# Kernel optimization log

Hardware: AMD Instinct MI355X
Metric: run time of the kernel (lower is better)

The kernel has to match this reference:

```python
import jax, jax.numpy as jnp
import numpy as np

N_NODES = 100000
N_EDGES = 1600000
D = 128


def _gine_layer(x, src, dst, e, W1, b1, W2, b2):
    # message: relu(x_j + e_ji), aggregate: sum at destination
    m = jax.nn.relu(x[src] + e)                       # [E, D]
    agg = jax.ops.segment_sum(m, dst, num_segments=x.shape[0])  # [N, D]
    h = agg + x                                       # (1 + eps) * x_i with eps = 0
    h = jax.nn.relu(jnp.dot(h, W1) + b1)
    return jnp.dot(h, W2) + b2


def setup_inputs() -> dict:
    key = jax.random.key(0)
    ks = jax.random.split(key, 16)
    s = 0.05
    inp = {
        "x": jax.random.normal(ks[0], (N_NODES, D), dtype=jnp.float32),
        "edge_index": jax.random.randint(ks[1], (2, N_EDGES), 0, N_NODES, dtype=jnp.int64) if jax.config.jax_enable_x64 else jax.random.randint(ks[1], (2, N_EDGES), 0, N_NODES, dtype=jnp.int32),
        "edge_attr": jax.random.randint(ks[2], (N_EDGES,), 0, 100, dtype=jnp.int32),
        "edge_emb": jax.random.normal(ks[3], (100, D), dtype=jnp.float32) * s,
        "Win": jax.random.normal(ks[4], (D, D), dtype=jnp.float32) * s,
        "b_in": jnp.zeros((D,), dtype=jnp.float32),
        "W1_0": jax.random.normal(ks[5], (D, D), dtype=jnp.float32) * s,
        "b1_0": jnp.zeros((D,), dtype=jnp.float32),
        "W2_0": jax.random.normal(ks[6], (D, D), dtype=jnp.float32) * s,
        "b2_0": jnp.zeros((D,), dtype=jnp.float32),
        "W1_1": jax.random.normal(ks[7], (D, D), dtype=jnp.float32) * s,
        "b1_1": jnp.zeros((D,), dtype=jnp.float32),
        "W2_1": jax.random.normal(ks[8], (D, D), dtype=jnp.float32) * s,
        "b2_1": jnp.zeros((D,), dtype=jnp.float32),
        "Wout": jax.random.normal(ks[9], (D, 1), dtype=jnp.float32) * s,
        "b_out": jnp.zeros((1,), dtype=jnp.float32),
    }
    return inp


def reference(x, edge_index, edge_attr, edge_emb, Win, b_in,
              W1_0, b1_0, W2_0, b2_0, W1_1, b1_1, W2_1, b2_1,
              Wout, b_out):
    src, dst = edge_index[0], edge_index[1]
    e = edge_emb[edge_attr]                 # [E, D] edge-attribute embedding lookup
    h = jnp.dot(x, Win) + b_in              # input_proj
    # layer 0: GINEConv + residual add + relu (norm=none, dropout off)
    h = jax.nn.relu(_gine_layer(h, src, dst, e, W1_0, b1_0, W2_0, b2_0) + h)
    # layer 1
    h = jax.nn.relu(_gine_layer(h, src, dst, e, W1_1, b1_1, W2_1, b2_1) + h)
    # output_mlp: single Linear(hidden, 1); no final activation, no pooling
    return jnp.dot(h, Wout) + b_out
```

## Files before the change

### kernel.cpp

```cpp
#include <hip/hip_runtime.h>

#define NN 100000
#define D 128
#define CHUNK 4096
#define BCSTRIDE 392

typedef __attribute__((ext_vector_type(8))) short short8;
typedef __attribute__((ext_vector_type(8))) unsigned short ushort8;
typedef __attribute__((ext_vector_type(4))) float f32x4;

__device__ __forceinline__ float4 ld4(const float* p) { return *(const float4*)p; }

__device__ __forceinline__ unsigned short f2bf(float f) {
    unsigned int u = __float_as_uint(f);
    unsigned int r = u + 0x7fffu + ((u >> 16) & 1u);
    return (unsigned short)(r >> 16);
}
__device__ __forceinline__ float bf2f(unsigned short h) {
    return __uint_as_float(((unsigned int)h) << 16);
}
__device__ __forceinline__ float blo(unsigned int u) { return __uint_as_float(u << 16); }
__device__ __forceinline__ float bhi(unsigned int u) { return __uint_as_float(u & 0xffff0000u); }

__device__ __forceinline__ int swz(int r, int c) {
    return r * 128 + ((((c >> 2) ^ (r & 7)) << 2) | (c & 3));
}

__device__ __forceinline__ void coop_gemm8(
    const unsigned int* uT,
    const unsigned short* __restrict__ Whi, const unsigned short* __restrict__ Wlo,
    int wv, int lane, int lr, int q, f32x4 acc[4])
{
    #pragma unroll
    for (int ks = 0; ks < 4; ++ks) {
        short8 ahi[4], alo[4];
        #pragma unroll
        for (int m = 0; m < 4; ++m) {
            const int row = m * 16 + lr;
            const int cb  = ks * 32 + q * 8;
            const uint4 a0 = *(const uint4*)&uT[swz(row, cb)];
            const uint4 a1 = *(const uint4*)&uT[swz(row, cb + 4)];
            const unsigned int w[8] = {a0.x, a0.y, a0.z, a0.w, a1.x, a1.y, a1.z, a1.w};
            #pragma unroll
            for (int j = 0; j < 8; ++j) {
                ahi[m][j] = (short)(w[j] >> 16);
                alo[m][j] = (short)(w[j] & 0xffffu);
            }
        }
        const int base = ((wv * 4 + ks) * 64 + lane) * 8;
        const short8 bhi8 = *(const short8*)&Whi[base];
        const short8 blo8 = *(const short8*)&Wlo[base];
        #pragma unroll
        for (int m = 0; m < 4; ++m) {
            acc[m] = __builtin_amdgcn_mfma_f32_16x16x32_bf16(alo[m], bhi8, acc[m], 0, 0, 0);
            acc[m] = __builtin_amdgcn_mfma_f32_16x16x32_bf16(ahi[m], blo8, acc[m], 0, 0, 0);
            acc[m] = __builtin_amdgcn_mfma_f32_16x16x32_bf16(ahi[m], bhi8, acc[m], 0, 0, 0);
        }
    }
}

__device__ __forceinline__ void gemm_in_body(
    unsigned int* uT, int bid,
    const float* __restrict__ A1,
    const unsigned short* __restrict__ Whi, const unsigned short* __restrict__ Wlo,
    const float* __restrict__ bias,
    unsigned short* __restrict__ out_hi, unsigned short* __restrict__ out_lo, int N)
{
    const int t    = threadIdx.x;
    const int wv   = t >> 6;
    const int lane = t & 63;
    const int lr   = lane & 15;
    const int q    = lane >> 4;
    const int rE   = wv * 8 + (lane >> 3);
    const int cE   = (lane & 7) * 16;
    const int rowE = bid * 64 + rE;

    {
        float v[16];
        if (rowE < N) {
            const int off = rowE * D + cE;
            #pragma unroll
            for (int k = 0; k < 4; ++k) {
                const float4 x = ld4(&A1[off + k * 4]);
                v[k * 4 + 0] = x.x; v[k * 4 + 1] = x.y; v[k * 4 + 2] = x.z; v[k * 4 + 3] = x.w;
            }
        } else {
            #pragma unroll
            for (int j = 0; j < 16; ++j) v[j] = 0.f;
        }
        #pragma unroll
        for (int k = 0; k < 4; ++k) {
            unsigned int pk[4];
            #pragma unroll
            for (int j = 0; j < 4; ++j) {
                const float f = v[k * 4 + j];
                const unsigned int hi = f2bf(f);
                pk[j] = (hi << 16) | f2bf(f - bf2f((unsigned short)hi));
            }
            *(uint4*)&uT[swz(rE, cE + k * 4)] = make_uint4(pk[0], pk[1], pk[2], pk[3]);
        }
    }
    __syncthreads();

    f32x4 acc[4];
    #pragma unroll
    for (int m = 0; m < 4; ++m) acc[m] = (f32x4){0.f, 0.f, 0.f, 0.f};
    coop_gemm8(uT, Whi, Wlo, wv, lane, lr, q, acc);
    __syncthreads();

    {
        const float b = bias[wv * 16 + lr];
        #pragma unroll
        for (int m = 0; m < 4; ++m)
            #pragma unroll
            for (int r = 0; r < 4; ++r)
                uT[swz(m * 16 + q * 4 + r, wv * 16 + lr)] = __float_as_uint(acc[m][r] + b);
    }
    __syncthreads();

    if (rowE < N) {
        const int off = rowE * D + cE;
        unsigned int w[16];
        #pragma unroll
        for (int k = 0; k < 4; ++k) {
            const uint4 a = *(const uint4*)&uT[swz(rE, cE + k * 4)];
            w[k * 4 + 0] = a.x; w[k * 4 + 1] = a.y; w[k * 4 + 2] = a.z; w[k * 4 + 3] = a.w;
        }
        #pragma unroll
        for (int h8 = 0; h8 < 2; ++h8) {
            ushort8 oh, ol;
            #pragma unroll
            for (int j = 0; j < 8; ++j) {
                const float o = __uint_as_float(w[h8 * 8 + j]);
                const unsigned short h = f2bf(o);
                oh[j] = h;
                ol[j] = f2bf(o - bf2f(h));
            }
            *(ushort8*)&out_hi[off + h8 * 8] = oh;
            *(ushort8*)&out_lo[off + h8 * 8] = ol;
        }
    }
}

__global__ __launch_bounds__(256) void setup_all(
    const float* __restrict__ W0, const float* __restrict__ W1,
    const float* __restrict__ W2, const float* __restrict__ W3,
    const float* __restrict__ W4, unsigned short* __restrict__ wp,
    const float* __restrict__ emb, unsigned int* __restrict__ embp,
    int* __restrict__ binTotal)
{
    const int T = blockIdx.x * 256 + threadIdx.x;
    if (T < 5 * D * D) {
        const int w = T / (D * D);
        const int t = T % (D * D);
        const float* W = (w == 0) ? W0 : (w == 1) ? W1 : (w == 2) ? W2 : (w == 3) ? W3 : W4;
        const int j  = t & 7;
        const int L  = (t >> 3) & 63;
        const int ks = (t >> 9) & 3;
        const int nt = t >> 11;
        const float v = W[(ks * 32 + (L >> 4) * 8 + j) * D + nt * 16 + (L & 15)];
        const unsigned short h = f2bf(v);
        unsigned short* hi = wp + (size_t)w * 2 * D * D;
        hi[t] = h;
        hi[D * D + t] = f2bf(v - bf2f(h));
    } else if (T < 5 * D * D + 6400) {
        const int i = T - 5 * D * D;
        embp[i] = (unsigned int)f2bf(emb[i * 2]) | ((unsigned int)f2bf(emb[i * 2 + 1]) << 16);
    } else if (T < 5 * D * D + 6400 + BCSTRIDE) {
        binTotal[T - 5 * D * D - 6400] = 0;
    }
}

__global__ __launch_bounds__(512, 8) void fuse_count_gemm(
    const int* __restrict__ dst, int* __restrict__ blkcnt,
    int* __restrict__ binTotal, int E, int nbins, int csrB,
    const float* __restrict__ A1,
    const unsigned short* __restrict__ Whi, const unsigned short* __restrict__ Wlo,
    const float* __restrict__ bias,
    unsigned short* __restrict__ out_hi, unsigned short* __restrict__ out_lo,
    int N, int gemmBase)
{
    __shared__ __align__(16) unsigned int uT[64 * 128];
    if ((int)blockIdx.x < csrB) {
        int* hist = (int*)uT;
        const int t = threadIdx.x;
        const int i = blockIdx.x;
        for (int k = t; k < nbins; k += 512) hist[k] = 0;
        __syncthreads();
        const int e0 = i * CHUNK;
        const int e1 = min(E, e0 + CHUNK);
        for (int e = e0 + t; e < e1; e += 512) atomicAdd(&hist[dst[e] >> 8], 1);
        __syncthreads();
        for (int k = t; k < nbins; k += 512) {
            const int c = hist[k];
            blkcnt[i * BCSTRIDE + k] = c;
            if (c) atomicAdd(&binTotal[k], c);
        }
    } else {
        gemm_in_body(uT, blockIdx.x - csrB + gemmBase, A1, Whi, Wlo, bias, out_hi, out_lo, N);
    }
}

__global__ __launch_bounds__(512) void bin_scan(
    const int* __restrict__ binTotal, int* __restrict__ binStart,
    int* __restrict__ binCursor, int nbins)
{
    __shared__ int s[512];
    const int t = threadIdx.x;
    const int v = (t < nbins) ? binTotal[t] : 0;
    s[t] = v;
    __syncthreads();
    for (int off = 1; off < 512; off <<= 1) {
        const int x = (t >= off) ? s[t - off] : 0;
        __syncthreads();
        s[t] += x;
        __syncthreads();
    }
    if (t < nbins) { binStart[t] = s[t] - v; binCursor[t] = s[t] - v; }
    if (t == 0)    binStart[nbins] = s[511];
}

__global__ __launch_bounds__(512, 8) void fuse_scatter_gemm(
    const int* __restrict__ src, const int* __restrict__ dst,
    const int* __restrict__ attr, const int* __restrict__ blkcnt,
    int* __restrict__ binCursor, int2* __restrict__ binned, int E, int nbins, int csrB,
    const float* __restrict__ A1,
    const unsigned short* __restrict__ Whi, const unsigned short* __restrict__ Wlo,
    const float* __restrict__ bias,
    unsigned short* __restrict__ out_hi, unsigned short* __restrict__ out_lo,
    int N, int gemmBase)
{
    __shared__ __align__(16) unsigned int uT[64 * 128];
    if ((int)blockIdx.x < csrB) {
        int* cur = (int*)uT;
        const int t = threadIdx.x;
        const int i = blockIdx.x;
        for (int k = t; k < nbins; k += 512) {
            const int c = blkcnt[i * BCSTRIDE + k];
            if (c) cur[k] = atomicAdd(&binCursor[k], c);
        }
        __syncthreads();
        const int e0 = i * CHUNK;
        const int e1 = min(E, e0 + CHUNK);
        for (int e = e0 + t; e < e1; e += 512) {
            const int d = dst[e];
            const int p = atomicAdd(&cur[d >> 8], 1);
            binned[p] = make_int2(src[e] | (attr[e] << 20), d);
        }
    } else {
        gemm_in_body(uT, blockIdx.x - csrB + gemmBase, A1, Whi, Wlo, bias, out_hi, out_lo, N);
    }
}

__global__ __launch_bounds__(512, 8) void fuse_build_gemm(
    const int2* __restrict__ binned, const int* __restrict__ binStart,
    int* __restrict__ rowptr, int* __restrict__ epack, int csrB,
    const float* __restrict__ A1,
    const unsigned short* __restrict__ Whi, const unsigned short* __restrict__ Wlo,
    const float* __restrict__ bias,
    unsigned short* __restrict__ out_hi, unsigned short* __restrict__ out_lo,
    int N, int gemmBase)
{
    __shared__ __align__(16) unsigned int uT[64 * 128];
    if ((int)blockIdx.x < csrB) {
        int* hist = (int*)uT;
        int* scn  = (int*)uT + 256;
        int* curn = (int*)uT + 512;
        const int t = threadIdx.x;
        const int b = blockIdx.x;
        if (t < 256) hist[t] = 0;
        __syncthreads();
        const int ebeg = binStart[b];
        const int eend = binStart[b + 1];
        for (int e = ebeg + t; e < eend; e += 512) atomicAdd(&hist[binned[e].y & 255], 1);
        __syncthreads();
        if (t < 256) scn[t] = hist[t];
        __syncthreads();
        for (int off = 1; off < 256; off <<= 1) {
            int x = 0;
            if (t < 256 && t >= off) x = scn[t - off];
            __syncthreads();
            if (t < 256) scn[t] += x;
            __syncthreads();
        }
        if (t < 256) {
            const int node = b * 256 + t;
            if (node < N) rowptr[node] = ebeg + scn[t];
            curn[t] = ebeg + scn[t] - hist[t];
        }
        __syncthreads();
        for (int e = ebeg + t; e < eend; e += 512) {
            const int2 v = binned[e];
            const int p = atomicAdd(&curn[v.y & 255], 1);
            epack[p] = v.x;
        }
    } else {
        gemm_in_body(uT, blockIdx.x - csrB + gemmBase, A1, Whi, Wlo, bias, out_hi, out_lo, N);
    }
}

template<bool LAST>
__global__ __launch_bounds__(512, 8) void gine_fused(
    const unsigned short* __restrict__ h_hi, const unsigned short* __restrict__ h_lo,
    const int* __restrict__ rowptr, const int* __restrict__ epack,
    const unsigned int* __restrict__ embp,
    const unsigned short* __restrict__ W1hi, const unsigned short* __restrict__ W1lo,
    const float* __restrict__ b1,
    const unsigned short* __restrict__ W2hi, const unsigned short* __restrict__ W2lo,
    const float* __restrict__ b2,
    unsigned short* __restrict__ out_hi, unsigned short* __restrict__ out_lo,
    const float* __restrict__ Wout, const float* __restrict__ bout,
    float* __restrict__ outv, int N)
{
    __shared__ __align__(16) unsigned int uT[64 * 128];
    const int t    = threadIdx.x;
    const int wv   = t >> 6;
    const int lane = t & 63;
    const int lr   = lane & 15;
    const int q    = lane >> 4;
    const int rE   = wv * 8 + (lane >> 3);
    const int cE   = (lane & 7) * 16;
    const int rowE = blockIdx.x * 64 + rE;

    const unsigned int* hu = (const unsigned int*)h_hi;

    for (int i = 0; i < 8; ++i) {
        const int row  = wv * 8 + i;
        const int node = blockIdx.x * 64 + row;
        if (node >= N) break;
        int start = (node == 0) ? 0 : rowptr[node - 1];
        int end   = rowptr[node];
        start = __builtin_amdgcn_readfirstlane(start);
        end   = __builtin_amdgcn_readfirstlane(end);

        float ax = 0.f, ay = 0.f;
        int j = start;

        for (; j < end && (j & 3); ++j) {
            const int p0 = __builtin_amdgcn_readfirstlane(epack[j]);
            const unsigned int u0 = hu[(p0 & 0xFFFFF) * 64 + lane];
            const unsigned int v0 = embp[(p0 >> 20) * 64 + lane];
            ax += fmaxf(blo(u0) + blo(v0), 0.f);
            ay += fmaxf(bhi(u0) + bhi(v0), 0.f);
        }

        for (; j + 7 < end; j += 8) {
            const int4 pk0 = *(const int4*)&epack[j];
            const int4 pk1 = *(const int4*)&epack[j + 4];
            int p[8];
            p[0] = __builtin_amdgcn_readfirstlane(pk0.x);
            p[1] = __builtin_amdgcn_readfirstlane(pk0.y);
            p[2] = __builtin_amdgcn_readfirstlane(pk0.z);
            p[3] = __builtin_amdgcn_readfirstlane(pk0.w);
            p[4] = __builtin_amdgcn_readfirstlane(pk1.x);
            p[5] = __builtin_amdgcn_readfirstlane(pk1.y);
            p[6] = __builtin_amdgcn_readfirstlane(pk1.z);
            p[7] = __builtin_amdgcn_readfirstlane(pk1.w);
            unsigned int u[8], v[8];
            #pragma unroll
            for (int k = 0; k < 8; ++k) u[k] = hu[(p[k] & 0xFFFFF) * 64 + lane];
            #pragma unroll
            for (int k = 0; k < 8; ++k) v[k] = embp[(p[k] >> 20) * 64 + lane];
            #pragma unroll
            for (int k = 0; k < 8; ++k) {
                ax += fmaxf(blo(u[k]) + blo(v[k]), 0.f);
                ay += fmaxf(bhi(u[k]) + bhi(v[k]), 0.f);
            }
        }

        if (j + 3 < end) {
            const int4 pk0 = *(const int4*)&epack[j];
            int p[4];
            p[0] = __builtin_amdgcn_readfirstlane(pk0.x);
            p[1] = __builtin_amdgcn_readfirstlane(pk0.y);
            p[2] = __builtin_amdgcn_readfirstlane(pk0.z);
            p[3] = __builtin_amdgcn_readfirstlane(pk0.w);
            unsigned int u[4], v[4];
            #pragma unroll
            for (int k = 0; k < 4; ++k) u[k] = hu[(p[k] & 0xFFFFF) * 64 + lane];
            #pragma unroll
            for (int k = 0; k < 4; ++k) v[k] = embp[(p[k] >> 20) * 64 + lane];
            #pragma unroll
            for (int k = 0; k < 4; ++k) {
                ax += fmaxf(blo(u[k]) + blo(v[k]), 0.f);
                ay += fmaxf(bhi(u[k]) + bhi(v[k]), 0.f);
            }
            j += 4;
        }

        for (; j < end; ++j) {
            const int p0 = __builtin_amdgcn_readfirstlane(epack[j]);
            const unsigned int u0 = hu[(p0 & 0xFFFFF) * 64 + lane];
            const unsigned int v0 = embp[(p0 >> 20) * 64 + lane];
            ax += fmaxf(blo(u0) + blo(v0), 0.f);
            ay += fmaxf(bhi(u0) + bhi(v0), 0.f);
        }

        *(float2*)&uT[swz(row, 2 * lane)] = make_float2(ax, ay);
    }

    {
        float v[16];
        if (rowE < N) {
            #pragma unroll
            for (int k = 0; k < 4; ++k) {
                const uint4 a = *(const uint4*)&uT[swz(rE, cE + k * 4)];
                v[k * 4 + 0] = __uint_as_float(a.x);
                v[k * 4 + 1] = __uint_as_float(a.y);
                v[k * 4 + 2] = __uint_as_float(a.z);
                v[k * 4 + 3] = __uint_as_float(a.w);
            }
            const int off = rowE * D + cE;
            #pragma unroll
            for (int h8 = 0; h8 < 2; ++h8) {
                const ushort8 hh = *(const ushort8*)&h_hi[off + h8 * 8];
                const ushort8 ll = *(const ushort8*)&h_lo[off + h8 * 8];
                #pragma unroll
                for (int j = 0; j < 8; ++j) v[h8 * 8 + j] += bf2f(hh[j]) + bf2f(ll[j]);
            }
        } else {
            #pragma unroll
            for (int j = 0; j < 16; ++j) v[j] = 0.f;
        }
        #pragma unroll
        for (int k = 0; k < 4; ++k) {
            unsigned int pk[4];
            #pragma unroll
            for (int j = 0; j < 4; ++j) {
                const float f = v[k * 4 + j];
                const unsigned int hi = f2bf(f);
                pk[j] = (hi << 16) | f2bf(f - bf2f((unsigned short)hi));
            }
            *(uint4*)&uT[swz(rE, cE + k * 4)] = make_uint4(pk[0], pk[1], pk[2], pk[3]);
        }
    }
    __syncthreads();

    f32x4 acc[4];
    #pragma unroll
    for (int m = 0; m < 4; ++m) acc[m] = (f32x4){0.f, 0.f, 0.f, 0.f};
    coop_gemm8(uT, W1hi, W1lo, wv, lane, lr, q, acc);
    __syncthreads();

    {
        const float b = b1[wv * 16 + lr];
        #pragma unroll
        for (int m = 0; m < 4; ++m)
            #pragma unroll
            for (int r = 0; r < 4; ++r) {
                const float o = fmaxf(acc[m][r] + b, 0.f);
                const unsigned int hi = f2bf(o);
                const unsigned int lo = f2bf(o - bf2f((unsigned short)hi));
                uT[swz(m * 16 + q * 4 + r, wv * 16 + lr)] = (hi << 16) | lo;
            }
    }
    __syncthreads();

    f32x4 acc2[4];
    #pragma unroll
    for (int m = 0; m < 4; ++m) acc2[m] = (f32x4){0.f, 0.f, 0.f, 0.f};
    coop_gemm8(uT, W2hi, W2lo, wv, lane, lr, q, acc2);
    __syncthreads();

    {
        const float b = b2[wv * 16 + lr];
        #pragma unroll
        for (int m = 0; m < 4; ++m)
            #pragma unroll
            for (int r = 0; r < 4; ++r)
                uT[swz(m * 16 + q * 4 + r, wv * 16 + lr)] = __float_as_uint(acc2[m][r] + b);
    }
    __syncthreads();

    if (LAST) {
        float accv = 0.f;
        if (rowE < N) {
            const int off = rowE * D + cE;
            unsigned int w[16];
            #pragma unroll
            for (int k = 0; k < 4; ++k) {
                const uint4 a = *(const uint4*)&uT[swz(rE, cE + k * 4)];
                w[k * 4 + 0] = a.x; w[k * 4 + 1] = a.y; w[k * 4 + 2] = a.z; w[k * 4 + 3] = a.w;
            }
            #pragma unroll
            for (int h8 = 0; h8 < 2; ++h8) {
                const ushort8 hh = *(const ushort8*)&h_hi[off + h8 * 8];
                const ushort8 ll = *(const ushort8*)&h_lo[off + h8 * 8];
                const float4 w0 = ld4(&Wout[cE + h8 * 8]);
                const float4 w1 = ld4(&Wout[cE + h8 * 8 + 4]);
                float o[8];
                #pragma unroll
                for (int j = 0; j < 8; ++j)
                    o[j] = fmaxf(__uint_as_float(w[h8 * 8 + j]) + bf2f(hh[j]) + bf2f(ll[j]), 0.f);
                accv += o[0] * w0.x + o[1] * w0.y + o[2] * w0.z + o[3] * w0.w;
                accv += o[4] * w1.x + o[5] * w1.y + o[6] * w1.z + o[7] * w1.w;
            }
        }
        accv += __shfl_xor(accv, 1);
        accv += __shfl_xor(accv, 2);
        accv += __shfl_xor(accv, 4);
        if ((lane & 7) == 0 && rowE < N) outv[rowE] = accv + bout[0];
    } else if (rowE < N) {
        const int off = rowE * D + cE;
        unsigned int w[16];
        #pragma unroll
        for (int k = 0; k < 4; ++k) {
            const uint4 a = *(const uint4*)&uT[swz(rE, cE + k * 4)];
            w[k * 4 + 0] = a.x; w[k * 4 + 1] = a.y; w[k * 4 + 2] = a.z; w[k * 4 + 3] = a.w;
        }
        #pragma unroll
        for (int h8 = 0; h8 < 2; ++h8) {
            const ushort8 hh = *(const ushort8*)&h_hi[off + h8 * 8];
            const ushort8 ll = *(const ushort8*)&h_lo[off + h8 * 8];
            ushort8 oh, ol;
            #pragma unroll
            for (int j = 0; j < 8; ++j) {
                const float o = fmaxf(__uint_as_float(w[h8 * 8 + j]) + bf2f(hh[j]) + bf2f(ll[j]), 0.f);
                const unsigned short h = f2bf(o);
                oh[j] = h;
                ol[j] = f2bf(o - bf2f(h));
            }
            *(ushort8*)&out_hi[off + h8 * 8] = oh;
            *(ushort8*)&out_lo[off + h8 * 8] = ol;
        }
    }
}

extern "C" void kernel_launch(void* const* d_in, const int* in_sizes, int n_in,
                              void* d_out, int out_size, void* d_ws, size_t ws_size,
                              hipStream_t stream)
{
    const float* x     = (const float*)d_in[0];
    const int*   ei    = (const int*)  d_in[1];
    const int*   attr  = (const int*)  d_in[2];
    const float* emb   = (const float*)d_in[3];
    const float* Win   = (const float*)d_in[4];
    const float* b_in  = (const float*)d_in[5];
    const float* W1_0  = (const float*)d_in[6];
    const float* b1_0  = (const float*)d_in[7];
    const float* W2_0  = (const float*)d_in[8];
    const float* b2_0  = (const float*)d_in[9];
    const float* W1_1  = (const float*)d_in[10];
    const float* b1_1  = (const float*)d_in[11];
    const float* W2_1  = (const float*)d_in[12];
    const float* b2_1  = (const float*)d_in[13];
    const float* Wout  = (const float*)d_in[14];
    const float* b_out = (const float*)d_in[15];
    float* out = (float*)d_out;

    const int N = NN;
    const int E = in_sizes[2];
    const int* srcp = ei;
    const int* dstp = ei + E;
    const int nbins = (N + 255) >> 8;
    const int eblocks = (E + CHUNK - 1) / CHUNK;

    unsigned short* h_hi = (unsigned short*)d_ws;
    unsigned short* h_lo = h_hi + (size_t)N * D;
    float* aggspace = (float*)(h_lo + (size_t)N * D);
    int*   rowptr = (int*)(aggspace + (size_t)N * D);
    int*   epack  = rowptr + N;
    unsigned short* wp = (unsigned short*)(epack + E);
    unsigned short* Whi[5], *Wlo[5];
    for (int i = 0; i < 5; ++i) {
        Whi[i] = wp + (size_t)i * 2 * D * D;
        Wlo[i] = Whi[i] + D * D;
    }
    unsigned int* embp = (unsigned int*)(wp + 5 * 2 * D * D);
    int2* binned    = (int2*)aggspace;
    int*  blkcnt    = (int*)(binned + E);
    int*  binTotal  = blkcnt + eblocks * BCSTRIDE;
    int*  binStart  = binTotal + BCSTRIDE;
    int*  binCursor = binStart + BCSTRIDE;
    unsigned short* hB_hi = (unsigned short*)aggspace;
    unsigned short* hB_lo = hB_hi + (size_t)N * D;

    const int fgrid = (N + 63) / 64;
    const int sgrid = (5 * D * D + 6400 + BCSTRIDE + 255) / 256;

    const int G1 = 200;
    const int G2 = 700;
    const int G3 = fgrid - G1 - G2;

    setup_all<<<sgrid, dim3(256), 0, stream>>>(Win, W1_0, W2_0, W1_1, W2_1, wp, emb, embp, binTotal);

    fuse_count_gemm<<<eblocks + G1, dim3(512), 0, stream>>>(
        dstp, blkcnt, binTotal, E, nbins, eblocks,
        x, Whi[0], Wlo[0], b_in, h_hi, h_lo, N, 0);
    bin_scan<<<1, 512, 0, stream>>>(binTotal, binStart, binCursor, nbins);
    fuse_scatter_gemm<<<eblocks + G2, dim3(512), 0, stream>>>(
        srcp, dstp, attr, blkcnt, binCursor, binned, E, nbins, eblocks,
        x, Whi[0], Wlo[0], b_in, h_hi, h_lo, N, G1);
    fuse_build_gemm<<<nbins + G3, dim3(512), 0, stream>>>(
        binned, binStart, rowptr, epack, nbins,
        x, Whi[0], Wlo[0], b_in, h_hi, h_lo, N, G1 + G2);

    gine_fused<false><<<fgrid, dim3(512), 0, stream>>>(
        h_hi, h_lo, rowptr, epack, embp,
        Whi[1], Wlo[1], b1_0, Whi[2], Wlo[2], b2_0,
        hB_hi, hB_lo, nullptr, nullptr, nullptr, N);

    gine_fused<true><<<fgrid, dim3(512), 0, stream>>>(
        hB_hi, hB_lo, rowptr, epack, embp,
        Whi[3], Wlo[3], b1_1, Whi[4], Wlo[4], b2_1,
        nullptr, nullptr, Wout, b_out, out, N);
}
```

Baseline: 397.3 us.

## Store split bf16 hi/lo planes separately in LDS and fuse self-add into aggregation

Shared memory now holds the activation tile as two separate bf16 planes (hi and lo) with an 8-element XOR swizzle instead of packed 32-bit hi|lo words. The MFMA operand loads become direct short8 reads, removing per-element shift/mask unpacking in the GEMM inner loop. The aggregation kernel also adds the node's own features and splits to hi/lo right after the per-row edge reduction, dropping an extra LDS round trip and sync pass. Epilogue stores become 16-bit scalar writes to two planes, which may raise LDS store instruction count and bank conflicts.

```diff
diff --git a/kernel.cpp b/kernel.cpp
--- a/kernel.cpp
+++ b/kernel.cpp
@@ -25,9 +25,12 @@
 __device__ __forceinline__ int swz(int r, int c) {
     return r * 128 + ((((c >> 2) ^ (r & 7)) << 2) | (c & 3));
 }
+__device__ __forceinline__ int pidx(int p, int r, int c) {
+    return p * 8192 + r * 128 + (((c >> 3) ^ (r & 7)) << 3) + (c & 7);
+}
 
 __device__ __forceinline__ void coop_gemm8(
-    const unsigned int* uT,
+    const unsigned short* Hs,
     const unsigned short* __restrict__ Whi, const unsigned short* __restrict__ Wlo,
     int wv, int lane, int lr, int q, f32x4 acc[4])
 {
@@ -37,15 +40,9 @@
         #pragma unroll
         for (int m = 0; m < 4; ++m) {
             const int row = m * 16 + lr;
-            const int cb  = ks * 32 + q * 8;
-            const uint4 a0 = *(const uint4*)&uT[swz(row, cb)];
-            const uint4 a1 = *(const uint4*)&uT[swz(row, cb + 4)];
-            const unsigned int w[8] = {a0.x, a0.y, a0.z, a0.w, a1.x, a1.y, a1.z, a1.w};
-            #pragma unroll
-            for (int j = 0; j < 8; ++j) {
-                ahi[m][j] = (short)(w[j] >> 16);
-                alo[m][j] = (short)(w[j] & 0xffffu);
-            }
+            const int c   = ks * 32 + q * 8;
+            ahi[m] = *(const short8*)&Hs[pidx(0, row, c)];
+            alo[m] = *(const short8*)&Hs[pidx(1, row, c)];
         }
         const int base = ((wv * 4 + ks) * 64 + lane) * 8;
         const short8 bhi8 = *(const short8*)&Whi[base];
@@ -60,7 +57,7 @@
 }
 
 __device__ __forceinline__ void gemm_in_body(
-    unsigned int* uT, int bid,
+    unsigned short* Hs, int bid,
     const float* __restrict__ A1,
     const unsigned short* __restrict__ Whi, const unsigned short* __restrict__ Wlo,
     const float* __restrict__ bias,
@@ -89,15 +86,17 @@
             for (int j = 0; j < 16; ++j) v[j] = 0.f;
         }
         #pragma unroll
-        for (int k = 0; k < 4; ++k) {
-            unsigned int pk[4];
-            #pragma unroll
-            for (int j = 0; j < 4; ++j) {
-                const float f = v[k * 4 + j];
-                const unsigned int hi = f2bf(f);
-                pk[j] = (hi << 16) | f2bf(f - bf2f((unsigned short)hi));
-            }
-            *(uint4*)&uT[swz(rE, cE + k * 4)] = make_uint4(pk[0], pk[1], pk[2], pk[3]);
+        for (int h8 = 0; h8 < 2; ++h8) {
+            ushort8 hv, lv;
+            #pragma unroll
+            for (int j = 0; j < 8; ++j) {
+                const float f = v[h8 * 8 + j];
+                const unsigned short hi = f2bf(f);
+                hv[j] = hi;
+                lv[j] = f2bf(f - bf2f(hi));
+            }
+            *(ushort8*)&Hs[pidx(0, rE, cE + h8 * 8)] = hv;
+            *(ushort8*)&Hs[pidx(1, rE, cE + h8 * 8)] = lv;
         }
     }
     __syncthreads();
@@ -105,9 +104,10 @@
     f32x4 acc[4];
     #pragma unroll
     for (int m = 0; m < 4; ++m) acc[m] = (f32x4){0.f, 0.f, 0.f, 0.f};
-    coop_gemm8(uT, Whi, Wlo, wv, lane, lr, q, acc);
-    __syncthreads();
-
+    coop_gemm8(Hs, Whi, Wlo, wv, lane, lr, q, acc);
+    __syncthreads();
+
+    unsigned int* uT = (unsigned int*)Hs;
     {
         const float b = bias[wv * 16 + lr];
         #pragma unroll
@@ -180,9 +180,9 @@
     unsigned short* __restrict__ out_hi, unsigned short* __restrict__ out_lo,
     int N, int gemmBase)
 {
-    __shared__ __align__(16) unsigned int uT[64 * 128];
+    __shared__ __align__(16) unsigned short Hs[2 * 64 * 128];
     if ((int)blockIdx.x < csrB) {
-        int* hist = (int*)uT;
+        int* hist = (int*)Hs;
         const int t = threadIdx.x;
         const int i = blockIdx.x;
         for (int k = t; k < nbins; k += 512) hist[k] = 0;
@@ -197,7 +197,7 @@
             if (c) atomicAdd(&binTotal[k], c);
         }
     } else {
-        gemm_in_body(uT, blockIdx.x - csrB + gemmBase, A1, Whi, Wlo, bias, out_hi, out_lo, N);
+        gemm_in_body(Hs, blockIdx.x - csrB + gemmBase, A1, Whi, Wlo, bias, out_hi, out_lo, N);
     }
 }
 
@@ -230,9 +230,9 @@
     unsigned short* __restrict__ out_hi, unsigned short* __restrict__ out_lo,
     int N, int gemmBase)
 {
-    __shared__ __align__(16) unsigned int uT[64 * 128];
+    __shared__ __align__(16) unsigned short Hs[2 * 64 * 128];
     if ((int)blockIdx.x < csrB) {
-        int* cur = (int*)uT;
+        int* cur = (int*)Hs;
         const int t = threadIdx.x;
         const int i = blockIdx.x;
         for (int k = t; k < nbins; k += 512) {
@@ -248,7 +248,7 @@
             binned[p] = make_int2(src[e] | (attr[e] << 20), d);
         }
     } else {
-        gemm_in_body(uT, blockIdx.x - csrB + gemmBase, A1, Whi, Wlo, bias, out_hi, out_lo, N);
+        gemm_in_body(Hs, blockIdx.x - csrB + gemmBase, A1, Whi, Wlo, bias, out_hi, out_lo, N);
     }
 }
 
@@ -261,11 +261,11 @@
     unsigned short* __restrict__ out_hi, unsigned short* __restrict__ out_lo,
     int N, int gemmBase)
 {
-    __shared__ __align__(16) unsigned int uT[64 * 128];
+    __shared__ __align__(16) unsigned short Hs[2 * 64 * 128];
     if ((int)blockIdx.x < csrB) {
-        int* hist = (int*)uT;
-        int* scn  = (int*)uT + 256;
-        int* curn = (int*)uT + 512;
+        int* hist = (int*)Hs;
+        int* scn  = (int*)Hs + 256;
+        int* curn = (int*)Hs + 512;
         const int t = threadIdx.x;
         const int b = blockIdx.x;
         if (t < 256) hist[t] = 0;
@@ -295,7 +295,7 @@
             epack[p] = v.x;
         }
     } else {
-        gemm_in_body(uT, blockIdx.x - csrB + gemmBase, A1, Whi, Wlo, bias, out_hi, out_lo, N);
+        gemm_in_body(Hs, blockIdx.x - csrB + gemmBase, A1, Whi, Wlo, bias, out_hi, out_lo, N);
     }
 }
 
@@ -312,7 +312,7 @@
     const float* __restrict__ Wout, const float* __restrict__ bout,
     float* __restrict__ outv, int N)
 {
-    __shared__ __align__(16) unsigned int uT[64 * 128];
+    __shared__ __align__(16) unsigned short Hs[2 * 64 * 128];
     const int t    = threadIdx.x;
     const int wv   = t >> 6;
     const int lane = t & 63;
@@ -323,6 +323,7 @@
     const int rowE = blockIdx.x * 64 + rE;
 
     const unsigned int* hu = (const unsigned int*)h_hi;
+    const unsigned int* hl = (const unsigned int*)h_lo;
 
     for (int i = 0; i < 8; ++i) {
         const int row  = wv * 8 + i;
@@ -396,62 +397,36 @@
             ay += fmaxf(bhi(u0) + bhi(v0), 0.f);
         }
 
-        *(float2*)&uT[swz(row, 2 * lane)] = make_float2(ax, ay);
-    }
-
-    {
-        float v[16];
-        if (rowE < N) {
-            #pragma unroll
-            for (int k = 0; k < 4; ++k) {
-                const uint4 a = *(const uint4*)&uT[swz(rE, cE + k * 4)];
-                v[k * 4 + 0] = __uint_as_float(a.x);
-                v[k * 4 + 1] = __uint_as_float(a.y);
-                v[k * 4 + 2] = __uint_as_float(a.z);
-                v[k * 4 + 3] = __uint_as_float(a.w);
-            }
-            const int off = rowE * D + cE;
-            #pragma unroll
-            for (int h8 = 0; h8 < 2; ++h8) {
-                const ushort8 hh = *(const ushort8*)&h_hi[off + h8 * 8];
-                const ushort8 ll = *(const ushort8*)&h_lo[off + h8 * 8];
-                #pragma unroll
-                for (int j = 0; j < 8; ++j) v[h8 * 8 + j] += bf2f(hh[j]) + bf2f(ll[j]);
-            }
-        } else {
-            #pragma unroll
-            for (int j = 0; j < 16; ++j) v[j] = 0.f;
-        }
-        #pragma unroll
-        for (int k = 0; k < 4; ++k) {
-            unsigned int pk[4];
-            #pragma unroll
-            for (int j = 0; j < 4; ++j) {
-                const float f = v[k * 4 + j];
-                const unsigned int hi = f2bf(f);
-                pk[j] = (hi << 16) | f2bf(f - bf2f((unsigned short)hi));
-            }
-            *(uint4*)&uT[swz(rE, cE + k * 4)] = make_uint4(pk[0], pk[1], pk[2], pk[3]);
-        }
+        const unsigned int uh = hu[node * 64 + lane];
+        const unsigned int ul = hl[node * 64 + lane];
+        const float vx = ax + blo(uh) + blo(ul);
+        const float vy = ay + bhi(uh) + bhi(ul);
+        const unsigned int hx = f2bf(vx), hy = f2bf(vy);
+        const unsigned int lx = f2bf(vx - bf2f((unsigned short)hx));
+        const unsigned int ly = f2bf(vy - bf2f((unsigned short)hy));
+        *(unsigned int*)&Hs[pidx(0, row, 2 * lane)] = hx | (hy << 16);
+        *(unsigned int*)&Hs[pidx(1, row, 2 * lane)] = lx | (ly << 16);
     }
     __syncthreads();
 
     f32x4 acc[4];
     #pragma unroll
     for (int m = 0; m < 4; ++m) acc[m] = (f32x4){0.f, 0.f, 0.f, 0.f};
-    coop_gemm8(uT, W1hi, W1lo, wv, lane, lr, q, acc);
+    coop_gemm8(Hs, W1hi, W1lo, wv, lane, lr, q, acc);
     __syncthreads();
 
     {
         const float b = b1[wv * 16 + lr];
+        const int col = wv * 16 + lr;
         #pragma unroll
         for (int m = 0; m < 4; ++m)
             #pragma unroll
             for (int r = 0; r < 4; ++r) {
+                const int row = m * 16 + q * 4 + r;
                 const float o = fmaxf(acc[m][r] + b, 0.f);
-                const unsigned int hi = f2bf(o);
-                const unsigned int lo = f2bf(o - bf2f((unsigned short)hi));
-                uT[swz(m * 16 + q * 4 + r, wv * 16 + lr)] = (hi << 16) | lo;
+                const unsigned short hi = f2bf(o);
+                Hs[pidx(0, row, col)] = hi;
+                Hs[pidx(1, row, col)] = f2bf(o - bf2f(hi));
             }
     }
     __syncthreads();
@@ -459,9 +434,10 @@
     f32x4 acc2[4];
     #pragma unroll
     for (int m = 0; m < 4; ++m) acc2[m] = (f32x4){0.f, 0.f, 0.f, 0.f};
-    coop_gemm8(uT, W2hi, W2lo, wv, lane, lr, q, acc2);
-    __syncthreads();
-
+    coop_gemm8(Hs, W2hi, W2lo, wv, lane, lr, q, acc2);
+    __syncthreads();
+
+    unsigned int* uT = (unsigned int*)Hs;
     {
         const float b = b2[wv * 16 + lr];
         #pragma unroll
```

New measurement: 393.3 us (median of 3 runs). About the same (-1.0%).
